# Optimization experiments

Measured on AMD Instinct MI355X. Metric: run time of the kernel, lower is better.

## Reference

```python
import jax, jax.numpy as jnp
import numpy as np

GROUP_SIZE = 16
MIN_SIGMA = 1e-4


def setup_inputs() -> dict:
    key = jax.random.key(0)
    k1, k2, k3 = jax.random.split(key, 3)
    B, N, M, F = 4, 8192, 4096, 64
    return {
        "point_cloud": jax.random.normal(k1, (B, 3, N), dtype=jnp.float32),
        "query_cloud": jax.random.normal(k2, (B, 3, M), dtype=jnp.float32),
        "point_features": jax.random.normal(k3, (B, F, N), dtype=jnp.float32),
        "temperature": jnp.asarray(1.0, dtype=jnp.float32),
    }


def reference(point_cloud, query_cloud, point_features, temperature):
    # point_cloud: (B,3,N), query_cloud: (B,3,M), point_features: (B,F,N)
    k = GROUP_SIZE
    # Pairwise squared distances (B, M, N): ||q||^2 + ||p||^2 - 2 q.p
    q_sq = jnp.sum(query_cloud ** 2, axis=1)              # (B, M)
    p_sq = jnp.sum(point_cloud ** 2, axis=1)              # (B, N)
    qp = jnp.einsum('bdm,bdn->bmn', query_cloud, point_cloud)
    d2 = q_sq[:, :, None] + p_sq[:, None, :] - 2.0 * qp   # (B, M, N)
    # k nearest neighbors per query
    _, idx = jax.lax.top_k(-d2, k)                         # (B, M, k)

    # Gather neighbor coords and features: (B, 3, M, k), (B, F, M, k)
    idx_b = idx[:, None, :, :]                             # (B,1,M,k)
    grouped_points = jnp.take_along_axis(
        point_cloud[:, :, None, :], jnp.broadcast_to(idx_b, (idx.shape[0], 3, idx.shape[1], k)), axis=3)
    grouped_features = jnp.take_along_axis(
        point_features[:, :, None, :],
        jnp.broadcast_to(idx_b, (idx.shape[0], point_features.shape[1], idx.shape[1], k)), axis=3)

    # Soft-projection weights
    sigma = jnp.maximum(temperature ** 2, jnp.asarray(MIN_SIGMA, dtype=temperature.dtype))
    deltas = grouped_points - query_cloud[:, :, :, None]   # (B,3,M,k)
    dist = jnp.sum(deltas ** 2, axis=1, keepdims=True) / sigma  # (B,1,M,k)
    weights = jax.nn.softmax(-dist, axis=3)                # (B,1,M,k)

    projected_points = jnp.sum(grouped_points * weights, axis=3)     # (B,3,M)
    propagated_features = jnp.sum(grouped_features * weights, axis=3)  # (B,F,M)
    return (projected_points, propagated_features)
```

## Files before the change

### kernel.cpp

```cpp
#include <hip/hip_runtime.h>


#define BB 4
#define NN 8192
#define MM 4096
#define FF 64
#define KK 16
#define CHUNK 2048
#define NCHUNK 4
#define QPW 4
#define WAVES 16
#define QPB 64
#define SCAP 48

__global__ __launch_bounds__(256) void transpose_feat(const float* __restrict__ pf,
                                                      float* __restrict__ pfT) {
    __shared__ float tile[64][65];
    const int b = blockIdx.y;
    const int n0 = blockIdx.x * 64;
    const int t = threadIdx.x;
    const int n = t & 63, fq = t >> 6;
#pragma unroll
    for (int i = 0; i < 16; ++i) {
        int f = fq * 16 + i;
        tile[f][n] = pf[(size_t)b * FF * NN + (size_t)f * NN + n0 + n];
    }
    __syncthreads();
    const int f2 = t & 63, nq = t >> 6;
#pragma unroll
    for (int i = 0; i < 16; ++i) {
        int nn = nq * 16 + i;
        pfT[(size_t)b * NN * FF + (size_t)(n0 + nn) * FF + f2] = tile[f2][nn];
    }
}

#define D2EXPR(PX, PY, PZ, Q)                                         \
    ({ float dx_ = (PX) - qx[Q], dy_ = (PY) - qy[Q], dz_ = (PZ) - qz[Q]; \
       fmaf(dx_, dx_, fmaf(dy_, dy_, dz_ * dz_)); })

#define SCAN_PT(PX, PY, PZ)                      \
    do {                                         \
        _Pragma("unroll")                        \
        for (int q = 0; q < QPW; ++q) {          \
            float d2_ = D2EXPR(PX, PY, PZ, q);   \
            mn[q] = fminf(mn[q], d2_);           \
        }                                        \
    } while (0)

#define PASSB_PT(PX, PY, PZ, PIDX)                                   \
    do {                                                             \
        _Pragma("unroll")                                            \
        for (int q = 0; q < QPW; ++q) {                              \
            float d2_ = D2EXPR(PX, PY, PZ, q);                       \
            if (d2_ <= thr[q]) {                                     \
                int pos_ = atomicAdd(&s_cnt[wave * QPW + q], 1);     \
                if (pos_ < SCAP) {                                   \
                    s_surv_d2[(wave * QPW + q) * SCAP + pos_] = d2_; \
                    s_surv_idx[(wave * QPW + q) * SCAP + pos_] = (PIDX); \
                }                                                    \
            }                                                        \
        }                                                            \
    } while (0)

#define LOAD_CHUNK(C)                                                          \
    do {                                                                       \
        for (int j_ = t; j_ < 3 * CHUNK / 4; j_ += 1024) {                     \
            int arr_ = j_ >> 9;                                                \
            int off_ = j_ & 511;                                               \
            float4 v_ = *reinterpret_cast<const float4*>(pcb + arr_ * NN +     \
                                                         (C) * CHUNK + off_ * 4); \
            *reinterpret_cast<float4*>(s_pts + arr_ * CHUNK + off_ * 4) = v_;  \
        }                                                                      \
    } while (0)

__global__ __launch_bounds__(1024) void soft_proj_kernel(
    const float* __restrict__ pc, const float* __restrict__ qc,
    const float* __restrict__ pf, const float* __restrict__ pfT,
    const float* __restrict__ temp, float* __restrict__ out, int useT) {
    __shared__ __align__(16) float s_pts[3 * CHUNK];
    __shared__ __align__(16) float s_pool[WAVES * QPW * SCAP * 2];
    __shared__ int s_cnt[WAVES * QPW];
    __shared__ float s_sel_d2[WAVES * QPW * KK];
    __shared__ int s_sel_idx[WAVES * QPW * KK];

    const int bid = blockIdx.x;
    const int b = bid >> 6;
    const int m0 = (bid & 63) * QPB;
    const int t = threadIdx.x;
    const int wave = t >> 6;
    const int lane = t & 63;

    const float* pcb = pc + (size_t)b * 3 * NN;
    const int mbase = m0 + wave * QPW;

    float qx[QPW], qy[QPW], qz[QPW];
#pragma unroll
    for (int q = 0; q < QPW; ++q) {
        int m = mbase + q;
        qx[q] = qc[(size_t)b * 3 * MM + m];
        qy[q] = qc[(size_t)b * 3 * MM + MM + m];
        qz[q] = qc[(size_t)b * 3 * MM + 2 * MM + m];
    }

    float mn[QPW];
#pragma unroll
    for (int q = 0; q < QPW; ++q) mn[q] = 3.0e38f;

    for (int c = 0; c < NCHUNK; ++c) {
        __syncthreads();
        LOAD_CHUNK(c);
        __syncthreads();
#pragma unroll
        for (int i = 0; i < CHUNK / 256; ++i) {
            int o = i * 256 + lane * 4;
            float4 x4 = *reinterpret_cast<const float4*>(s_pts + o);
            float4 y4 = *reinterpret_cast<const float4*>(s_pts + CHUNK + o);
            float4 z4 = *reinterpret_cast<const float4*>(s_pts + 2 * CHUNK + o);
            SCAN_PT(x4.x, y4.x, z4.x);
            SCAN_PT(x4.y, y4.y, z4.y);
            SCAN_PT(x4.z, y4.z, z4.z);
            SCAN_PT(x4.w, y4.w, z4.w);
        }
    }

    float thr[QPW];
    {
        int rank[QPW] = {0, 0, 0, 0};
        for (int j = 0; j < 64; ++j) {
#pragma unroll
            for (int q = 0; q < QPW; ++q) {
                float mj = __shfl(mn[q], j, 64);
                rank[q] += (mj < mn[q] || (mj == mn[q] && j < lane)) ? 1 : 0;
            }
        }
#pragma unroll
        for (int q = 0; q < QPW; ++q) {
            unsigned long long bal = __ballot(rank[q] == 15);
            int src = __ffsll((unsigned long long)bal) - 1;
            thr[q] = __shfl(mn[q], src, 64);
        }
    }

    if (lane < QPW) s_cnt[wave * QPW + lane] = 0;

    float* s_surv_d2 = s_pool;
    int* s_surv_idx = (int*)(s_pool + WAVES * QPW * SCAP);

    for (int c = 0; c < NCHUNK; ++c) {
        __syncthreads();
        LOAD_CHUNK(c);
        __syncthreads();
#pragma unroll
        for (int i = 0; i < CHUNK / 256; ++i) {
            int o = i * 256 + lane * 4;
            float4 x4 = *reinterpret_cast<const float4*>(s_pts + o);
            float4 y4 = *reinterpret_cast<const float4*>(s_pts + CHUNK + o);
            float4 z4 = *reinterpret_cast<const float4*>(s_pts + 2 * CHUNK + o);
            int gb = c * CHUNK + o;
            PASSB_PT(x4.x, y4.x, z4.x, gb + 0);
            PASSB_PT(x4.y, y4.y, z4.y, gb + 1);
            PASSB_PT(x4.z, y4.z, z4.z, gb + 2);
            PASSB_PT(x4.w, y4.w, z4.w, gb + 3);
        }
    }
    __syncthreads();

#pragma unroll
    for (int q = 0; q < QPW; ++q) {
        int wq = wave * QPW + q;
        int cnt = s_cnt[wq];
        if (cnt > SCAP) cnt = SCAP;
        if (lane < cnt) {
            float dv = s_surv_d2[wq * SCAP + lane];
            int iv = s_surv_idx[wq * SCAP + lane];
            int rank = 0;
            for (int j = 0; j < cnt; ++j) {
                float dj = s_surv_d2[wq * SCAP + j];
                int ij = s_surv_idx[wq * SCAP + j];
                rank += (dj < dv || (dj == dv && ij < iv)) ? 1 : 0;
            }
            if (rank < KK) {
                s_sel_d2[wq * KK + rank] = dv;
                s_sel_idx[wq * KK + rank] = iv;
            }
        }
    }
    __syncthreads();

    float* stage = s_pool;
    float tval = temp[0];
    float sigma = fmaxf(tval * tval, 1.0e-4f);
    float inv_sigma = 1.0f / sigma;
    const float* pfTb = pfT + (size_t)b * NN * FF;
    const float* pfb = pf + (size_t)b * FF * NN;

#pragma unroll
    for (int q = 0; q < QPW; ++q) {
        int wq = wave * QPW + q;
        int qm = wq & 63;
        float dk[KK];
        int ik[KK];
#pragma unroll
        for (int k = 0; k < KK; ++k) {
            dk[k] = s_sel_d2[wq * KK + k];
            ik[k] = __builtin_amdgcn_readfirstlane(s_sel_idx[wq * KK + k]);
        }
        float dmin = dk[0];
#pragma unroll
        for (int k = 1; k < KK; ++k) dmin = fminf(dmin, dk[k]);
        float ek[KK];
        float ssum = 0.f;
#pragma unroll
        for (int k = 0; k < KK; ++k) {
            ek[k] = __expf((dmin - dk[k]) * inv_sigma);
            ssum += ek[k];
        }
        float rs = 1.0f / ssum;

        float fv[KK];
        if (useT) {
#pragma unroll
            for (int k = 0; k < KK; ++k) fv[k] = pfTb[(size_t)ik[k] * FF + lane];
        } else {
#pragma unroll
            for (int k = 0; k < KK; ++k) fv[k] = pfb[(size_t)lane * NN + ik[k]];
        }
        float acc = 0.f;
#pragma unroll
        for (int k = 0; k < KK; ++k) acc = fmaf(ek[k], fv[k], acc);
        stage[lane * 65 + qm] = acc * rs;

        float px = 0.f, py = 0.f, pz = 0.f;
        if (lane < KK) {
            float dd = s_sel_d2[wq * KK + lane];
            int ii = s_sel_idx[wq * KK + lane];
            float e = __expf((dmin - dd) * inv_sigma);
            px = pcb[ii] * e;
            py = pcb[NN + ii] * e;
            pz = pcb[2 * NN + ii] * e;
        }
#pragma unroll
        for (int off = 1; off < KK; off <<= 1) {
            px += __shfl_xor(px, off, 64);
            py += __shfl_xor(py, off, 64);
            pz += __shfl_xor(pz, off, 64);
        }
        if (lane == 0) {
            stage[(64 + 0) * 65 + qm] = px * rs;
            stage[(64 + 1) * 65 + qm] = py * rs;
            stage[(64 + 2) * 65 + qm] = pz * rs;
        }
    }
    __syncthreads();

    const size_t featOff = (size_t)BB * 3 * MM;
    for (int j = t; j < 67 * 64; j += 1024) {
        int row = j >> 6, col = j & 63;
        float v = stage[row * 65 + col];
        int m = m0 + col;
        if (row < 64)
            out[featOff + (size_t)b * FF * MM + (size_t)row * MM + m] = v;
        else
            out[(size_t)b * 3 * MM + (size_t)(row - 64) * MM + m] = v;
    }
}

extern "C" void kernel_launch(void* const* d_in, const int* in_sizes, int n_in,
                              void* d_out, int out_size, void* d_ws, size_t ws_size,
                              hipStream_t stream) {
    (void)in_sizes; (void)n_in; (void)out_size;
    const float* pc = (const float*)d_in[0];
    const float* qc = (const float*)d_in[1];
    const float* pf = (const float*)d_in[2];
    const float* temp = (const float*)d_in[3];
    float* out = (float*)d_out;
    float* pfT = (float*)d_ws;
    const size_t needT = (size_t)BB * NN * FF * sizeof(float);
    int useT = (ws_size >= needT && d_ws != nullptr) ? 1 : 0;

    if (useT) {
        hipLaunchKernelGGL(transpose_feat, dim3(NN / 64, BB), dim3(256), 0, stream,
                           pf, pfT);
    }
    hipLaunchKernelGGL(soft_proj_kernel, dim3((BB * MM) / QPB), dim3(1024), 0,
                       stream, pc, qc, pf, pfT, temp, out, useT);
}
```

Before: 142.0 us.

## Use expanded-distance scan, split points across wave halves, radix-select threshold

Rewrites the kNN scan to compute -2q·p + |p|^2 with precomputed point norms staged in shared memory. Each wave now handles 8 queries over half of each chunk, so query registers get more reuse. The rank-based threshold selection is replaced by a ballot-driven bitwise radix search on order-preserving float keys. The two halves' thresholds are merged with a max, and exact distances are recomputed from gathered coordinates in the epilogue. This cuts ALU work per point pair and the cost of threshold selection. The trade-offs are more register pressure, a coarser threshold that can admit more survivors into a bounded buffer, and possible precision differences from the expanded-distance form.

```diff
diff --git a/kernel.cpp b/kernel.cpp
--- a/kernel.cpp
+++ b/kernel.cpp
@@ -8,10 +8,10 @@
 #define KK 16
 #define CHUNK 2048
 #define NCHUNK 4
-#define QPW 4
-#define WAVES 16
+#define QPW 8
 #define QPB 64
-#define SCAP 48
+#define SCAP 54
+#define NTHR 1024
 
 __global__ __launch_bounds__(256) void transpose_feat(const float* __restrict__ pf,
                                                       float* __restrict__ pfT) {
@@ -29,59 +29,60 @@
     const int f2 = t & 63, nq = t >> 6;
 #pragma unroll
     for (int i = 0; i < 16; ++i) {
-        int nn = nq * 16 + i;
-        pfT[(size_t)b * NN * FF + (size_t)(n0 + nn) * FF + f2] = tile[f2][nn];
-    }
-}
-
-#define D2EXPR(PX, PY, PZ, Q)                                         \
-    ({ float dx_ = (PX) - qx[Q], dy_ = (PY) - qy[Q], dz_ = (PZ) - qz[Q]; \
-       fmaf(dx_, dx_, fmaf(dy_, dy_, dz_ * dz_)); })
-
-#define SCAN_PT(PX, PY, PZ)                      \
-    do {                                         \
-        _Pragma("unroll")                        \
-        for (int q = 0; q < QPW; ++q) {          \
-            float d2_ = D2EXPR(PX, PY, PZ, q);   \
-            mn[q] = fminf(mn[q], d2_);           \
-        }                                        \
+        int nn2 = nq * 16 + i;
+        pfT[(size_t)b * NN * FF + (size_t)(n0 + nn2) * FF + f2] = tile[f2][nn2];
+    }
+}
+
+__device__ __forceinline__ unsigned mapf(float f) {
+    unsigned u = __float_as_uint(f);
+    return (u & 0x80000000u) ? ~u : (u | 0x80000000u);
+}
+__device__ __forceinline__ float unmapf(unsigned k) {
+    return (k & 0x80000000u) ? __uint_as_float(k ^ 0x80000000u)
+                             : __uint_as_float(~k);
+}
+
+#define STAGE(C)                                                            \
+    do {                                                                    \
+        if (t < CHUNK / 4) {                                                \
+            int base_ = (C)*CHUNK + t * 4;                                  \
+            float4 x4_ = *(const float4*)(pcb + base_);                     \
+            float4 y4_ = *(const float4*)(pcb + NN + base_);                \
+            float4 z4_ = *(const float4*)(pcb + 2 * NN + base_);            \
+            *(float4*)(s_pts + t * 4) = x4_;                                \
+            *(float4*)(s_pts + CHUNK + t * 4) = y4_;                        \
+            *(float4*)(s_pts + 2 * CHUNK + t * 4) = z4_;                    \
+            float4 p4_;                                                     \
+            p4_.x = fmaf(x4_.x, x4_.x, fmaf(y4_.x, y4_.x, z4_.x * z4_.x));  \
+            p4_.y = fmaf(x4_.y, x4_.y, fmaf(y4_.y, y4_.y, z4_.y * z4_.y));  \
+            p4_.z = fmaf(x4_.z, x4_.z, fmaf(y4_.z, y4_.z, z4_.z * z4_.z));  \
+            p4_.w = fmaf(x4_.w, x4_.w, fmaf(y4_.w, y4_.w, z4_.w * z4_.w));  \
+            *(float4*)(s_pts + 3 * CHUNK + t * 4) = p4_;                    \
+        }                                                                   \
     } while (0)
 
-#define PASSB_PT(PX, PY, PZ, PIDX)                                   \
-    do {                                                             \
-        _Pragma("unroll")                                            \
-        for (int q = 0; q < QPW; ++q) {                              \
-            float d2_ = D2EXPR(PX, PY, PZ, q);                       \
-            if (d2_ <= thr[q]) {                                     \
-                int pos_ = atomicAdd(&s_cnt[wave * QPW + q], 1);     \
-                if (pos_ < SCAP) {                                   \
-                    s_surv_d2[(wave * QPW + q) * SCAP + pos_] = d2_; \
-                    s_surv_idx[(wave * QPW + q) * SCAP + pos_] = (PIDX); \
-                }                                                    \
-            }                                                        \
-        }                                                            \
+#define VAL(X, Y, Z, PS, Q) \
+    fmaf((X), qx2[Q], fmaf((Y), qy2[Q], fmaf((Z), qz2[Q], (PS))))
+
+#define PUSH(WQ, V, I)                                          \
+    do {                                                        \
+        int pos_ = atomicAdd(&s_cnt[WQ], 1);                    \
+        if (pos_ < SCAP) {                                      \
+            s_surv[((WQ)*SCAP + pos_) * 2] = (V);               \
+            s_surv[((WQ)*SCAP + pos_) * 2 + 1] = __int_as_float(I); \
+        }                                                       \
     } while (0)
 
-#define LOAD_CHUNK(C)                                                          \
-    do {                                                                       \
-        for (int j_ = t; j_ < 3 * CHUNK / 4; j_ += 1024) {                     \
-            int arr_ = j_ >> 9;                                                \
-            int off_ = j_ & 511;                                               \
-            float4 v_ = *reinterpret_cast<const float4*>(pcb + arr_ * NN +     \
-                                                         (C) * CHUNK + off_ * 4); \
-            *reinterpret_cast<float4*>(s_pts + arr_ * CHUNK + off_ * 4) = v_;  \
-        }                                                                      \
-    } while (0)
-
-__global__ __launch_bounds__(1024) void soft_proj_kernel(
+__global__ __launch_bounds__(NTHR, 4) void soft_proj_kernel(
     const float* __restrict__ pc, const float* __restrict__ qc,
     const float* __restrict__ pf, const float* __restrict__ pfT,
     const float* __restrict__ temp, float* __restrict__ out, int useT) {
-    __shared__ __align__(16) float s_pts[3 * CHUNK];
-    __shared__ __align__(16) float s_pool[WAVES * QPW * SCAP * 2];
-    __shared__ int s_cnt[WAVES * QPW];
-    __shared__ float s_sel_d2[WAVES * QPW * KK];
-    __shared__ int s_sel_idx[WAVES * QPW * KK];
+    __shared__ __align__(16) float s_pts[4 * CHUNK];
+    __shared__ __align__(16) float s_surv[QPB * SCAP * 2];
+    __shared__ int s_cnt[QPB];
+    __shared__ int s_sel[QPB * KK];
+    __shared__ float s_thr[2 * QPB];
 
     const int bid = blockIdx.x;
     const int b = bid >> 6;
@@ -89,17 +90,19 @@
     const int t = threadIdx.x;
     const int wave = t >> 6;
     const int lane = t & 63;
+    const int pairIdx = wave & 7;
+    const int half = wave >> 3;
 
     const float* pcb = pc + (size_t)b * 3 * NN;
-    const int mbase = m0 + wave * QPW;
-
-    float qx[QPW], qy[QPW], qz[QPW];
+    const float* qcb = qc + (size_t)b * 3 * MM;
+
+    float qx2[QPW], qy2[QPW], qz2[QPW];
 #pragma unroll
     for (int q = 0; q < QPW; ++q) {
-        int m = mbase + q;
-        qx[q] = qc[(size_t)b * 3 * MM + m];
-        qy[q] = qc[(size_t)b * 3 * MM + MM + m];
-        qz[q] = qc[(size_t)b * 3 * MM + 2 * MM + m];
+        int m = m0 + pairIdx * QPW + q;
+        qx2[q] = -2.0f * qcb[m];
+        qy2[q] = -2.0f * qcb[MM + m];
+        qz2[q] = -2.0f * qcb[2 * MM + m];
     }
 
     float mn[QPW];
@@ -108,86 +111,104 @@
 
     for (int c = 0; c < NCHUNK; ++c) {
         __syncthreads();
-        LOAD_CHUNK(c);
-        __syncthreads();
-#pragma unroll
-        for (int i = 0; i < CHUNK / 256; ++i) {
-            int o = i * 256 + lane * 4;
-            float4 x4 = *reinterpret_cast<const float4*>(s_pts + o);
-            float4 y4 = *reinterpret_cast<const float4*>(s_pts + CHUNK + o);
-            float4 z4 = *reinterpret_cast<const float4*>(s_pts + 2 * CHUNK + o);
-            SCAN_PT(x4.x, y4.x, z4.x);
-            SCAN_PT(x4.y, y4.y, z4.y);
-            SCAN_PT(x4.z, y4.z, z4.z);
-            SCAN_PT(x4.w, y4.w, z4.w);
-        }
-    }
-
-    float thr[QPW];
-    {
-        int rank[QPW] = {0, 0, 0, 0};
-        for (int j = 0; j < 64; ++j) {
+        STAGE(c);
+        __syncthreads();
+        const int ob = half * 1024 + lane * 4;
+#pragma unroll
+        for (int g = 0; g < 4; ++g) {
+            int oo = ob + g * 256;
+            float4 x4 = *(const float4*)(s_pts + oo);
+            float4 y4 = *(const float4*)(s_pts + CHUNK + oo);
+            float4 z4 = *(const float4*)(s_pts + 2 * CHUNK + oo);
+            float4 p4 = *(const float4*)(s_pts + 3 * CHUNK + oo);
 #pragma unroll
             for (int q = 0; q < QPW; ++q) {
-                float mj = __shfl(mn[q], j, 64);
-                rank[q] += (mj < mn[q] || (mj == mn[q] && j < lane)) ? 1 : 0;
+                float v0 = VAL(x4.x, y4.x, z4.x, p4.x, q);
+                float v1 = VAL(x4.y, y4.y, z4.y, p4.y, q);
+                float v2 = VAL(x4.z, y4.z, z4.z, p4.z, q);
+                float v3 = VAL(x4.w, y4.w, z4.w, p4.w, q);
+                mn[q] = fminf(mn[q], fminf(fminf(v0, v1), fminf(v2, v3)));
             }
         }
-#pragma unroll
-        for (int q = 0; q < QPW; ++q) {
-            unsigned long long bal = __ballot(rank[q] == 15);
-            int src = __ffsll((unsigned long long)bal) - 1;
-            thr[q] = __shfl(mn[q], src, 64);
-        }
-    }
-
-    if (lane < QPW) s_cnt[wave * QPW + lane] = 0;
-
-    float* s_surv_d2 = s_pool;
-    int* s_surv_idx = (int*)(s_pool + WAVES * QPW * SCAP);
+    }
+
+    float thrv[QPW];
+#pragma unroll
+    for (int q = 0; q < QPW; ++q) {
+        unsigned key = mapf(mn[q]);
+        unsigned res = 0u;
+        for (int bb = 31; bb >= 8; --bb) {
+            unsigned cand = res | (1u << bb);
+            unsigned long long bal = __ballot(key < cand);
+            int c2 = __popcll(bal);
+            if (c2 < 8) res = cand;
+        }
+        thrv[q] = unmapf(res | 0xFFu);
+    }
+    if (lane == 0) {
+#pragma unroll
+        for (int q = 0; q < QPW; ++q)
+            s_thr[half * QPB + pairIdx * QPW + q] = thrv[q];
+    }
+    if (t < QPB) s_cnt[t] = 0;
+    __syncthreads();
+#pragma unroll
+    for (int q = 0; q < QPW; ++q)
+        thrv[q] = fmaxf(s_thr[pairIdx * QPW + q], s_thr[QPB + pairIdx * QPW + q]);
 
     for (int c = 0; c < NCHUNK; ++c) {
         __syncthreads();
-        LOAD_CHUNK(c);
-        __syncthreads();
-#pragma unroll
-        for (int i = 0; i < CHUNK / 256; ++i) {
-            int o = i * 256 + lane * 4;
-            float4 x4 = *reinterpret_cast<const float4*>(s_pts + o);
-            float4 y4 = *reinterpret_cast<const float4*>(s_pts + CHUNK + o);
-            float4 z4 = *reinterpret_cast<const float4*>(s_pts + 2 * CHUNK + o);
-            int gb = c * CHUNK + o;
-            PASSB_PT(x4.x, y4.x, z4.x, gb + 0);
-            PASSB_PT(x4.y, y4.y, z4.y, gb + 1);
-            PASSB_PT(x4.z, y4.z, z4.z, gb + 2);
-            PASSB_PT(x4.w, y4.w, z4.w, gb + 3);
-        }
-    }
-    __syncthreads();
-
-#pragma unroll
-    for (int q = 0; q < QPW; ++q) {
-        int wq = wave * QPW + q;
+        STAGE(c);
+        __syncthreads();
+        const int ob = half * 1024 + lane * 4;
+#pragma unroll
+        for (int g = 0; g < 4; ++g) {
+            int oo = ob + g * 256;
+            float4 x4 = *(const float4*)(s_pts + oo);
+            float4 y4 = *(const float4*)(s_pts + CHUNK + oo);
+            float4 z4 = *(const float4*)(s_pts + 2 * CHUNK + oo);
+            float4 p4 = *(const float4*)(s_pts + 3 * CHUNK + oo);
+            int gi = c * CHUNK + oo;
+#pragma unroll
+            for (int q = 0; q < QPW; ++q) {
+                int wqq = pairIdx * QPW + q;
+                float v0 = VAL(x4.x, y4.x, z4.x, p4.x, q);
+                float v1 = VAL(x4.y, y4.y, z4.y, p4.y, q);
+                float v2 = VAL(x4.z, y4.z, z4.z, p4.z, q);
+                float v3 = VAL(x4.w, y4.w, z4.w, p4.w, q);
+                if (v0 <= thrv[q]) PUSH(wqq, v0, gi + 0);
+                if (v1 <= thrv[q]) PUSH(wqq, v1, gi + 1);
+                if (v2 <= thrv[q]) PUSH(wqq, v2, gi + 2);
+                if (v3 <= thrv[q]) PUSH(wqq, v3, gi + 3);
+            }
+        }
+    }
+    __syncthreads();
+
+#pragma unroll
+    for (int qq = 0; qq < 4; ++qq) {
+        int wq = wave * 4 + qq;
         int cnt = s_cnt[wq];
+        cnt = __builtin_amdgcn_readfirstlane(cnt);
         if (cnt > SCAP) cnt = SCAP;
-        if (lane < cnt) {
-            float dv = s_surv_d2[wq * SCAP + lane];
-            int iv = s_surv_idx[wq * SCAP + lane];
-            int rank = 0;
-            for (int j = 0; j < cnt; ++j) {
-                float dj = s_surv_d2[wq * SCAP + j];
-                int ij = s_surv_idx[wq * SCAP + j];
-                rank += (dj < dv || (dj == dv && ij < iv)) ? 1 : 0;
-            }
-            if (rank < KK) {
-                s_sel_d2[wq * KK + rank] = dv;
-                s_sel_idx[wq * KK + rank] = iv;
-            }
-        }
-    }
-    __syncthreads();
-
-    float* stage = s_pool;
+        bool valid = lane < cnt;
+        float mv = 0.f;
+        int mi = 0;
+        if (valid) {
+            mv = s_surv[(wq * SCAP + lane) * 2];
+            mi = __float_as_int(s_surv[(wq * SCAP + lane) * 2 + 1]);
+        }
+        int rank = 0;
+        for (int j = 0; j < cnt; ++j) {
+            float vj = s_surv[(wq * SCAP + j) * 2];
+            int ij = __float_as_int(s_surv[(wq * SCAP + j) * 2 + 1]);
+            if (valid && (vj < mv || (vj == mv && ij < mi))) rank++;
+        }
+        if (valid && rank < KK) s_sel[wq * KK + rank] = mi;
+    }
+    __syncthreads();
+
+    float* stage = s_surv;
     float tval = temp[0];
     float sigma = fmaxf(tval * tval, 1.0e-4f);
     float inv_sigma = 1.0f / sigma;
@@ -195,66 +216,48 @@
     const float* pfb = pf + (size_t)b * FF * NN;
 
 #pragma unroll
-    for (int q = 0; q < QPW; ++q) {
-        int wq = wave * QPW + q;
-        int qm = wq & 63;
+    for (int qq = 0; qq < 4; ++qq) {
+        int wq = wave * 4 + qq;
+        int m = m0 + wq;
+        float qxe = qcb[m], qye = qcb[MM + m], qze = qcb[2 * MM + m];
+        int ik[KK];
         float dk[KK];
-        int ik[KK];
 #pragma unroll
         for (int k = 0; k < KK; ++k) {
-            dk[k] = s_sel_d2[wq * KK + k];
-            ik[k] = __builtin_amdgcn_readfirstlane(s_sel_idx[wq * KK + k]);
+            int ii = __builtin_amdgcn_readfirstlane(s_sel[wq * KK + k]);
+            ik[k] = ii;
+            float px = pcb[ii], py = pcb[NN + ii], pz = pcb[2 * NN + ii];
+            float dx = px - qxe, dy = py - qye, dz = pz - qze;
+            dk[k] = fmaf(dx, dx, fmaf(dy, dy, dz * dz));
         }
         float dmin = dk[0];
 #pragma unroll
         for (int k = 1; k < KK; ++k) dmin = fminf(dmin, dk[k]);
-        float ek[KK];
-        float ssum = 0.f;
+        float ssum = 0.f, facc = 0.f, sx = 0.f, sy = 0.f, sz = 0.f;
 #pragma unroll
         for (int k = 0; k < KK; ++k) {
-            ek[k] = __expf((dmin - dk[k]) * inv_sigma);
-            ssum += ek[k];
+            float e = __expf((dmin - dk[k]) * inv_sigma);
+            ssum += e;
+            float px = pcb[ik[k]], py = pcb[NN + ik[k]], pz = pcb[2 * NN + ik[k]];
+            sx = fmaf(e, px, sx);
+            sy = fmaf(e, py, sy);
+            sz = fmaf(e, pz, sz);
+            float fv = useT ? pfTb[(size_t)ik[k] * FF + lane]
+                            : pfb[(size_t)lane * NN + ik[k]];
+            facc = fmaf(e, fv, facc);
         }
         float rs = 1.0f / ssum;
-
-        float fv[KK];
-        if (useT) {
-#pragma unroll
-            for (int k = 0; k < KK; ++k) fv[k] = pfTb[(size_t)ik[k] * FF + lane];
-        } else {
-#pragma unroll
-            for (int k = 0; k < KK; ++k) fv[k] = pfb[(size_t)lane * NN + ik[k]];
-        }
-        float acc = 0.f;
-#pragma unroll
-        for (int k = 0; k < KK; ++k) acc = fmaf(ek[k], fv[k], acc);
-        stage[lane * 65 + qm] = acc * rs;
-
-        float px = 0.f, py = 0.f, pz = 0.f;
-        if (lane < KK) {
-            float dd = s_sel_d2[wq * KK + lane];
-            int ii = s_sel_idx[wq * KK + lane];
-            float e = __expf((dmin - dd) * inv_sigma);
-            px = pcb[ii] * e;
-            py = pcb[NN + ii] * e;
-            pz = pcb[2 * NN + ii] * e;
-        }
-#pragma unroll
-        for (int off = 1; off < KK; off <<= 1) {
-            px += __shfl_xor(px, off, 64);
-            py += __shfl_xor(py, off, 64);
-            pz += __shfl_xor(pz, off, 64);
-        }
+        stage[lane * 65 + wq] = facc * rs;
         if (lane == 0) {
-            stage[(64 + 0) * 65 + qm] = px * rs;
-            stage[(64 + 1) * 65 + qm] = py * rs;
-            stage[(64 + 2) * 65 + qm] = pz * rs;
+            stage[64 * 65 + wq] = sx * rs;
+            stage[65 * 65 + wq] = sy * rs;
+            stage[66 * 65 + wq] = sz * rs;
         }
     }
     __syncthreads();
 
     const size_t featOff = (size_t)BB * 3 * MM;
-    for (int j = t; j < 67 * 64; j += 1024) {
+    for (int j = t; j < 67 * 64; j += NTHR) {
         int row = j >> 6, col = j & 63;
         float v = stage[row * 65 + col];
         int m = m0 + col;
@@ -282,6 +285,6 @@
         hipLaunchKernelGGL(transpose_feat, dim3(NN / 64, BB), dim3(256), 0, stream,
                            pf, pfT);
     }
-    hipLaunchKernelGGL(soft_proj_kernel, dim3((BB * MM) / QPB), dim3(1024), 0,
+    hipLaunchKernelGGL(soft_proj_kernel, dim3((BB * MM) / QPB), dim3(NTHR), 0,
                        stream, pc, qc, pf, pfT, temp, out, useT);
 }
```

New measurement: 131.9 us. -7.1%, faster.
